# Optimization experiments

Measured on AMD Instinct MI355X. Metric: run time of the kernel, lower is better.

The kernel has to match this reference:

```python
import jax, jax.numpy as jnp
import numpy as np


def setup_inputs() -> dict:
    key = jax.random.key(0)
    k1, k2, k3, k4, k5 = jax.random.split(key, 5)
    B, H, W, C = 4, 64, 64, 512
    ratio = 8
    d = C // ratio  # 64
    x = jax.random.normal(k1, (B, H, W, C), dtype=jnp.float32)
    # 1x1 conv weights (no bias) == channel-mixing matrices, he_normal-ish scale
    Wq = jax.random.normal(k2, (C, d), dtype=jnp.float32) * np.sqrt(2.0 / C)
    Wk = jax.random.normal(k3, (C, d), dtype=jnp.float32) * np.sqrt(2.0 / C)
    Wv = jax.random.normal(k4, (C, C), dtype=jnp.float32) * np.sqrt(2.0 / C)
    gamma = jax.random.normal(k5, (1,), dtype=jnp.float32)
    return {"x": x, "Wq": Wq, "Wk": Wk, "Wv": Wv, "gamma": gamma}


def reference(x, Wq, Wk, Wv, gamma):
    B, H, W, C = x.shape
    N = H * W
    # 1x1 convs (no bias) are per-pixel channel matmuls
    q = jnp.einsum('bhwc,cd->bhwd', x, Wq).reshape(B, N, -1)  # [B,N,d]
    k = jnp.einsum('bhwc,cd->bhwd', x, Wk).reshape(B, N, -1)  # [B,N,d]
    v = jnp.einsum('bhwc,cd->bhwd', x, Wv).reshape(B, N, C)   # [B,N,C]
    # energy[b,i,j] = key_i . query_j  (batch_dot(key, query^T))
    energy = jnp.einsum('bid,bjd->bij', k, q)                 # [B,N,N]
    attn = jax.nn.softmax(energy, axis=-1)
    out = jnp.einsum('bij,bjc->bic', attn, v)                 # [B,N,C]
    out = out.reshape(B, H, W, C)
    return gamma * out
```

## Files before the change

### kernel.cpp

```cpp
#include <hip/hip_runtime.h>
#include <hip/hip_bf16.h>

typedef unsigned short u16;
typedef unsigned int   u32;
typedef __attribute__((ext_vector_type(8))) short short8;
typedef __attribute__((ext_vector_type(4))) float f32x4;
typedef __attribute__((ext_vector_type(4))) u16   u16x4;

#define MFMA16(a,b,c) __builtin_amdgcn_mfma_f32_16x16x32_bf16((a),(b),(c),0,0,0)

#define BATCH 4
#define NPIX  4096
#define CCH   512
#define DDIM  64
#define MFIX  64.0f

static __device__ __forceinline__ u16 f2bf(float f){
  __hip_bfloat16 h = __float2bfloat16(f);
  return __builtin_bit_cast(u16, h);
}
static __device__ __forceinline__ float bf2f(u16 u){
  __hip_bfloat16 h = __builtin_bit_cast(__hip_bfloat16, u);
  return __bfloat162float(h);
}

__global__ __launch_bounds__(256) void k_wconv(const f32x4* __restrict__ wv,
                                               u16x4* __restrict__ wvb){
  const int i = blockIdx.x*256 + threadIdx.x;
  #pragma unroll
  for (int it=0; it<4; ++it){
    int idx = i + it*16384;
    f32x4 v = wv[idx];
    u16x4 o;
    o[0]=f2bf(v[0]); o[1]=f2bf(v[1]); o[2]=f2bf(v[2]); o[3]=f2bf(v[3]);
    wvb[idx] = o;
  }
}

__global__ __launch_bounds__(256) void k_qkproj(const float* __restrict__ x,
                                                const float* __restrict__ Wq,
                                                const float* __restrict__ Wk,
                                                u16* __restrict__ qhi, u16* __restrict__ qlo,
                                                u16* __restrict__ khi, u16* __restrict__ klo,
                                                u16* __restrict__ xhi){
  __shared__ float xs[32][512];
  const int pix0 = blockIdx.x * 32;
  {
    const f32x4* xg = (const f32x4*)(x + (size_t)pix0*CCH);
    f32x4* xsv = (f32x4*)(&xs[0][0]);
    #pragma unroll
    for (int it=0; it<16; ++it) xsv[threadIdx.x + it*256] = xg[threadIdx.x + it*256];
  }
  __syncthreads();
  #pragma unroll
  for (int e=0; e<16; ++e){
    int idx4 = e*256 + threadIdx.x;
    int f = idx4*4;
    int row = f >> 9, col = f & 511;
    f32x4 v = *(const f32x4*)(&xs[row][col]);
    u16x4 o;
    o[0]=f2bf(v[0]); o[1]=f2bf(v[1]); o[2]=f2bf(v[2]); o[3]=f2bf(v[3]);
    *(u16x4*)(&xhi[(size_t)(pix0+row)*CCH + col]) = o;
  }
  const int col = threadIdx.x & 127;
  const int grp = threadIdx.x >> 7;
  const float* W = (col < 64) ? Wq : Wk;
  const int wc = col & 63;
  float acc[16];
  #pragma unroll
  for (int p=0;p<16;++p) acc[p] = 0.f;
  #pragma unroll 2
  for (int c=0;c<512;c+=4){
    float w0 = W[(c+0)*64 + wc];
    float w1 = W[(c+1)*64 + wc];
    float w2 = W[(c+2)*64 + wc];
    float w3 = W[(c+3)*64 + wc];
    #pragma unroll
    for (int p=0;p<16;++p){
      f32x4 xv = *(const f32x4*)(&xs[grp*16+p][c]);
      acc[p] += xv[0]*w0 + xv[1]*w1 + xv[2]*w2 + xv[3]*w3;
    }
  }
  #pragma unroll
  for (int p=0;p<16;++p){
    int pix = pix0 + grp*16 + p;
    float v = acc[p];
    u16 hi = f2bf(v);
    u16 lo = f2bf(v - bf2f(hi));
    if (col < 64){ qhi[pix*64+wc] = hi; qlo[pix*64+wc] = lo; }
    else         { khi[pix*64+wc] = hi; klo[pix*64+wc] = lo; }
  }
}

__global__ __launch_bounds__(256) void k_vproj(const u16* __restrict__ xhi,
                                               const u16* __restrict__ wvb,
                                               u16* __restrict__ vT){
  __shared__ u16 As[64][72];
  __shared__ u16 Bs[64][266];
  const int pix0 = blockIdx.x * 64;
  const int c0   = blockIdx.y * 256;
  const int tid = threadIdx.x;
  const int w = tid >> 6, l = tid & 63;
  const int lg = l >> 4, ll = l & 15;
  f32x4 acc[4][4];
  #pragma unroll
  for (int mf=0;mf<4;++mf)
    #pragma unroll
    for (int nf=0;nf<4;++nf){ f32x4 z = {0.f,0.f,0.f,0.f}; acc[mf][nf] = z; }

  for (int ks=0; ks<8; ++ks){
    __syncthreads();
    #pragma unroll
    for (int it=0; it<2; ++it){
      int ch = tid + it*256; int r = ch>>3, c8 = ch&7;
      *(uint4*)(&As[r][c8*8]) = *(const uint4*)(&xhi[(size_t)(pix0+r)*CCH + ks*64 + c8*8]);
    }
    #pragma unroll
    for (int it=0; it<8; ++it){
      int ch = tid + it*256; int r = ch>>5, c32 = ch&31;
      uint4 d = *(const uint4*)(&wvb[(size_t)(ks*64+r)*CCH + c0 + c32*8]);
      u32* dst = (u32*)(&Bs[r][c32*8]);
      dst[0]=d.x; dst[1]=d.y; dst[2]=d.z; dst[3]=d.w;
    }
    __syncthreads();
    #pragma unroll
    for (int kc=0;kc<2;++kc){
      short8 a[4];
      #pragma unroll
      for (int mf=0;mf<4;++mf) a[mf] = *(const short8*)(&As[mf*16 + ll][kc*32 + lg*8]);
      #pragma unroll
      for (int nf=0;nf<4;++nf){
        short8 bb;
        int cc = w*64 + nf*16 + ll;
        #pragma unroll
        for (int e=0;e<8;++e) bb[e] = (short)Bs[kc*32 + lg*8 + e][cc];
        #pragma unroll
        for (int mf=0;mf<4;++mf) acc[mf][nf] = MFMA16(a[mf], bb, acc[mf][nf]);
      }
    }
  }
  #pragma unroll
  for (int mf=0;mf<4;++mf){
    #pragma unroll
    for (int nf=0;nf<4;++nf){
      int pix = pix0 + mf*16 + lg*4;
      int c   = c0 + w*64 + nf*16 + ll;
      u16x4 o;
      #pragma unroll
      for (int r=0;r<4;++r) o[r] = f2bf(acc[mf][nf][r]);
      size_t off = ((size_t)((pix>>12)*CCH + c))*NPIX + (pix & 4095);
      *(u16x4*)(vT + off) = o;
    }
  }
}

__global__ __launch_bounds__(512,2)
void k_attn(const u16* __restrict__ qhi, const u16* __restrict__ qlo,
            const u16* __restrict__ khi, const u16* __restrict__ klo,
            const u16* __restrict__ vT,  const float* __restrict__ gamma_p,
            float* __restrict__ out){
  __shared__ u16 Ps[2][128][72];
  __shared__ u16 Qs[2][64][72];
  const int bid = blockIdx.x;
  const int x  = bid & 7;
  const int b  = x >> 1, ch = x & 1;
  const int i0 = (bid >> 3) * 128;
  const int tid = threadIdx.x;
  const int w = tid >> 6, l = tid & 63;
  const int lg = l >> 4, ll = l & 15;
  const int irow0 = (w >> 2) * 64;
  const int cw    = ch*256 + (w & 3) * 64;

  const u16* qh_b  = qhi + (size_t)b*NPIX*DDIM;
  const u16* ql_b  = qlo + (size_t)b*NPIX*DDIM;
  const u16* vbase = vT  + (size_t)b*CCH*NPIX;

  short8 kfh[2], kfl[2];
  #pragma unroll
  for (int kc=0;kc<2;++kc){
    size_t a = ((size_t)(b*NPIX + i0 + w*16 + ll))*DDIM + kc*32 + lg*8;
    kfh[kc] = *(const short8*)(khi + a);
    kfl[kc] = *(const short8*)(klo + a);
  }
  short8 ones;
  #pragma unroll
  for (int e=0;e<8;++e) ones[e] = (short)0x3F80;

  f32x4 acc[4][4];
  #pragma unroll
  for (int mf=0;mf<4;++mf)
    #pragma unroll
    for (int nf=0;nf<4;++nf){ f32x4 z = {0.f,0.f,0.f,0.f}; acc[mf][nf] = z; }
  f32x4 accl[4];
  #pragma unroll
  for (int mf=0;mf<4;++mf){ f32x4 z = {0.f,0.f,0.f,0.f}; accl[mf] = z; }

  const int sc0   = tid*2;
  const int spart = sc0 >> 9;
  const int srow  = (sc0 >> 3) & 63;
  const int sq    = sc0 & 7;
  const u16* sgl  = spart ? ql_b : qh_b;
  uint4 qr0, qr1;

  auto stage_load = [&](int j0){
    const u16* p = sgl + (size_t)(j0 + srow)*DDIM + sq*8;
    qr0 = *(const uint4*)p;
    qr1 = *(const uint4*)(p + 8);
  };
  auto stage_write = [&](){
    u16* d = &Qs[spart][srow][sq*8];
    *(uint4*)d       = qr0;
    *(uint4*)(d + 8) = qr1;
  };

  auto s_step = [&](int buf){
    f32x4 s[4];
    #pragma unroll
    for (int jf=0;jf<4;++jf){ f32x4 z = {0.f,0.f,0.f,0.f}; s[jf] = z; }
    #pragma unroll
    for (int kc=0;kc<2;++kc){
      #pragma unroll
      for (int jf=0;jf<4;++jf){
        short8 qh = *(const short8*)(&Qs[0][jf*16 + ll][kc*32 + lg*8]);
        short8 qv = *(const short8*)(&Qs[1][jf*16 + ll][kc*32 + lg*8]);
        s[jf] = MFMA16(kfh[kc], qh, s[jf]);
        s[jf] = MFMA16(kfl[kc], qh, s[jf]);
        s[jf] = MFMA16(kfh[kc], qv, s[jf]);
      }
    }
    #pragma unroll
    for (int jf=0;jf<4;++jf)
      #pragma unroll
      for (int r=0;r<4;++r)
        Ps[buf][w*16 + lg*4 + r][jf*16 + ll] = f2bf(__expf(s[jf][r] - MFIX));
  };

  stage_load(0);
  stage_write();
  stage_load(64);
  __syncthreads();
  s_step(0);

  for (int t=0; t<64; ++t){
    const int j0 = t*64;

    short8 vb[8];
    #pragma unroll
    for (int kc=0;kc<2;++kc)
      #pragma unroll
      for (int nf=0;nf<4;++nf)
        vb[kc*4+nf] = *(const short8*)(vbase + (size_t)(cw + nf*16 + ll)*NPIX + j0 + kc*32 + lg*8);

    __syncthreads();
    if (t < 63){
      stage_write();
      if (t < 62) stage_load(j0 + 128);
    }
    __syncthreads();
    if (t < 63) s_step((t+1)&1);

    #pragma unroll
    for (int kc=0;kc<2;++kc){
      short8 pa[4];
      #pragma unroll
      for (int mf=0;mf<4;++mf) pa[mf] = *(const short8*)(&Ps[t&1][irow0 + mf*16 + ll][kc*32 + lg*8]);
      #pragma unroll
      for (int nf=0;nf<4;++nf)
        #pragma unroll
        for (int mf=0;mf<4;++mf) acc[mf][nf] = MFMA16(pa[mf], vb[kc*4+nf], acc[mf][nf]);
      #pragma unroll
      for (int mf=0;mf<4;++mf) accl[mf] = MFMA16(pa[mf], ones, accl[mf]);
    }
  }

  const float gm = gamma_p[0];
  #pragma unroll
  for (int mf=0;mf<4;++mf){
    f32x4 inv;
    #pragma unroll
    for (int r=0;r<4;++r) inv[r] = gm / accl[mf][r];
    #pragma unroll
    for (int nf=0;nf<4;++nf)
      #pragma unroll
      for (int r=0;r<4;++r){
        int row = i0 + irow0 + mf*16 + lg*4 + r;
        int c   = cw + nf*16 + ll;
        out[((size_t)(b*NPIX + row))*CCH + c] = acc[mf][nf][r] * inv[r];
      }
  }
}

extern "C" void kernel_launch(void* const* d_in, const int* in_sizes, int n_in,
                              void* d_out, int out_size, void* d_ws, size_t ws_size,
                              hipStream_t stream) {
  (void)in_sizes; (void)n_in; (void)out_size; (void)ws_size;
  const float* x  = (const float*)d_in[0];
  const float* Wq = (const float*)d_in[1];
  const float* Wk = (const float*)d_in[2];
  const float* Wv = (const float*)d_in[3];
  const float* gm = (const float*)d_in[4];
  float* out = (float*)d_out;

  u16* qhi = (u16*)d_ws;
  u16* qlo = qhi + (size_t)BATCH*NPIX*DDIM;
  u16* khi = qlo + (size_t)BATCH*NPIX*DDIM;
  u16* klo = khi + (size_t)BATCH*NPIX*DDIM;
  u16* vT  = klo + (size_t)BATCH*NPIX*DDIM;

  u16* xhi = (u16*)d_out;
  u16* wvb = xhi + (size_t)BATCH*NPIX*CCH;

  k_qkproj<<<dim3(512), dim3(256), 0, stream>>>(x, Wq, Wk, qhi, qlo, khi, klo, xhi);
  k_wconv<<<dim3(64), dim3(256), 0, stream>>>((const f32x4*)Wv, (u16x4*)wvb);
  k_vproj<<<dim3(256,2), dim3(256), 0, stream>>>(xhi, wvb, vT);
  k_attn<<<dim3(256), dim3(512), 0, stream>>>(qhi, qlo, khi, klo, vT, gm, out);
}
```

Measured before the change: 246.3 us.

## Halve attention row tile to 64 and redistribute warps for more blocks

The attention kernel now handles 64 query rows per block instead of 128, doubling the grid to 512 blocks and raising the launch-bounds occupancy target to 4. Each wave computes a 16x32 slice of the score tile, with the Q/K operand roles swapped so the P tile is written with vector stores. Each wave also covers 32 output channels instead of 64. The aim is better CU fill and latency hiding on a 256-CU device. The cost is that each V tile is reused over fewer rows, so total V traffic doubles, and the tighter register budget may cause spills.

```diff
diff --git a/kernel.cpp b/kernel.cpp
--- a/kernel.cpp
+++ b/kernel.cpp
@@ -154,22 +154,23 @@
   }
 }
 
-__global__ __launch_bounds__(512,2)
+__global__ __launch_bounds__(512,4)
 void k_attn(const u16* __restrict__ qhi, const u16* __restrict__ qlo,
             const u16* __restrict__ khi, const u16* __restrict__ klo,
             const u16* __restrict__ vT,  const float* __restrict__ gamma_p,
             float* __restrict__ out){
-  __shared__ u16 Ps[2][128][72];
+  __shared__ u16 Ps[2][64][72];
   __shared__ u16 Qs[2][64][72];
   const int bid = blockIdx.x;
   const int x  = bid & 7;
   const int b  = x >> 1, ch = x & 1;
-  const int i0 = (bid >> 3) * 128;
+  const int i0 = (bid >> 3) * 64;
   const int tid = threadIdx.x;
   const int w = tid >> 6, l = tid & 63;
   const int lg = l >> 4, ll = l & 15;
-  const int irow0 = (w >> 2) * 64;
-  const int cw    = ch*256 + (w & 3) * 64;
+  const int iw = (w & 3) * 16;
+  const int jw = (w >> 2) * 32;
+  const int cw = ch*256 + w*32;
 
   const u16* qh_b  = qhi + (size_t)b*NPIX*DDIM;
   const u16* ql_b  = qlo + (size_t)b*NPIX*DDIM;
@@ -178,7 +179,7 @@
   short8 kfh[2], kfl[2];
   #pragma unroll
   for (int kc=0;kc<2;++kc){
-    size_t a = ((size_t)(b*NPIX + i0 + w*16 + ll))*DDIM + kc*32 + lg*8;
+    size_t a = ((size_t)(b*NPIX + i0 + iw + ll))*DDIM + kc*32 + lg*8;
     kfh[kc] = *(const short8*)(khi + a);
     kfl[kc] = *(const short8*)(klo + a);
   }
@@ -186,11 +187,11 @@
   #pragma unroll
   for (int e=0;e<8;++e) ones[e] = (short)0x3F80;
 
-  f32x4 acc[4][4];
+  f32x4 acc[4][2];
   #pragma unroll
   for (int mf=0;mf<4;++mf)
     #pragma unroll
-    for (int nf=0;nf<4;++nf){ f32x4 z = {0.f,0.f,0.f,0.f}; acc[mf][nf] = z; }
+    for (int nf=0;nf<2;++nf){ f32x4 z = {0.f,0.f,0.f,0.f}; acc[mf][nf] = z; }
   f32x4 accl[4];
   #pragma unroll
   for (int mf=0;mf<4;++mf){ f32x4 z = {0.f,0.f,0.f,0.f}; accl[mf] = z; }
@@ -214,25 +215,22 @@
   };
 
   auto s_step = [&](int buf){
-    f32x4 s[4];
-    #pragma unroll
-    for (int jf=0;jf<4;++jf){ f32x4 z = {0.f,0.f,0.f,0.f}; s[jf] = z; }
-    #pragma unroll
-    for (int kc=0;kc<2;++kc){
-      #pragma unroll
-      for (int jf=0;jf<4;++jf){
-        short8 qh = *(const short8*)(&Qs[0][jf*16 + ll][kc*32 + lg*8]);
-        short8 qv = *(const short8*)(&Qs[1][jf*16 + ll][kc*32 + lg*8]);
-        s[jf] = MFMA16(kfh[kc], qh, s[jf]);
-        s[jf] = MFMA16(kfl[kc], qh, s[jf]);
-        s[jf] = MFMA16(kfh[kc], qv, s[jf]);
+    #pragma unroll
+    for (int jf=0;jf<2;++jf){
+      f32x4 s = {0.f,0.f,0.f,0.f};
+      #pragma unroll
+      for (int kc=0;kc<2;++kc){
+        short8 qh = *(const short8*)(&Qs[0][jw + jf*16 + ll][kc*32 + lg*8]);
+        short8 ql = *(const short8*)(&Qs[1][jw + jf*16 + ll][kc*32 + lg*8]);
+        s = MFMA16(qh, kfh[kc], s);
+        s = MFMA16(ql, kfh[kc], s);
+        s = MFMA16(qh, kfl[kc], s);
       }
-    }
-    #pragma unroll
-    for (int jf=0;jf<4;++jf)
-      #pragma unroll
-      for (int r=0;r<4;++r)
-        Ps[buf][w*16 + lg*4 + r][jf*16 + ll] = f2bf(__expf(s[jf][r] - MFIX));
+      u16x4 pk;
+      #pragma unroll
+      for (int r=0;r<4;++r) pk[r] = f2bf(__expf(s[r] - MFIX));
+      *(u16x4*)(&Ps[buf][iw + ll][jw + jf*16 + lg*4]) = pk;
+    }
   };
 
   stage_load(0);
@@ -244,12 +242,12 @@
   for (int t=0; t<64; ++t){
     const int j0 = t*64;
 
-    short8 vb[8];
+    short8 vb[4];
     #pragma unroll
     for (int kc=0;kc<2;++kc)
       #pragma unroll
-      for (int nf=0;nf<4;++nf)
-        vb[kc*4+nf] = *(const short8*)(vbase + (size_t)(cw + nf*16 + ll)*NPIX + j0 + kc*32 + lg*8);
+      for (int nf=0;nf<2;++nf)
+        vb[kc*2+nf] = *(const short8*)(vbase + (size_t)(cw + nf*16 + ll)*NPIX + j0 + kc*32 + lg*8);
 
     __syncthreads();
     if (t < 63){
@@ -263,11 +261,11 @@
     for (int kc=0;kc<2;++kc){
       short8 pa[4];
       #pragma unroll
-      for (int mf=0;mf<4;++mf) pa[mf] = *(const short8*)(&Ps[t&1][irow0 + mf*16 + ll][kc*32 + lg*8]);
-      #pragma unroll
-      for (int nf=0;nf<4;++nf)
+      for (int mf=0;mf<4;++mf) pa[mf] = *(const short8*)(&Ps[t&1][mf*16 + ll][kc*32 + lg*8]);
+      #pragma unroll
+      for (int nf=0;nf<2;++nf)
         #pragma unroll
-        for (int mf=0;mf<4;++mf) acc[mf][nf] = MFMA16(pa[mf], vb[kc*4+nf], acc[mf][nf]);
+        for (int mf=0;mf<4;++mf) acc[mf][nf] = MFMA16(pa[mf], vb[kc*2+nf], acc[mf][nf]);
       #pragma unroll
       for (int mf=0;mf<4;++mf) accl[mf] = MFMA16(pa[mf], ones, accl[mf]);
     }
@@ -280,10 +278,10 @@
     #pragma unroll
     for (int r=0;r<4;++r) inv[r] = gm / accl[mf][r];
     #pragma unroll
-    for (int nf=0;nf<4;++nf)
+    for (int nf=0;nf<2;++nf)
       #pragma unroll
       for (int r=0;r<4;++r){
-        int row = i0 + irow0 + mf*16 + lg*4 + r;
+        int row = i0 + mf*16 + lg*4 + r;
         int c   = cw + nf*16 + ll;
         out[((size_t)(b*NPIX + row))*CCH + c] = acc[mf][nf][r] * inv[r];
       }
@@ -313,5 +311,5 @@
   k_qkproj<<<dim3(512), dim3(256), 0, stream>>>(x, Wq, Wk, qhi, qlo, khi, klo, xhi);
   k_wconv<<<dim3(64), dim3(256), 0, stream>>>((const f32x4*)Wv, (u16x4*)wvb);
   k_vproj<<<dim3(256,2), dim3(256), 0, stream>>>(xhi, wvb, vT);
-  k_attn<<<dim3(256), dim3(512), 0, stream>>>(qhi, qlo, khi, klo, vT, gm, out);
-}
+  k_attn<<<dim3(512), dim3(512), 0, stream>>>(qhi, qlo, khi, klo, vT, gm, out);
+}
```

After: 235.1 us. 4.6% less time.
